# Kernel tuning notes

Hardware: AMD Instinct MI355X
Metric: run time of the kernel (lower is better)

Reference implementation:

```python
import jax, jax.numpy as jnp
import numpy as np

B = 4096
N_FEAT = 4
VOCAB = 100000
EMB = 64
N_NEG = 3
TEMP = 1.0
EPS = 1e-8  # torch.cosine_similarity eps


def setup_inputs() -> dict:
    key = jax.random.key(0)
    ks = jax.random.split(key, 12)
    inp = {}
    inp['user_ids'] = jax.random.randint(ks[0], (B, N_FEAT), 0, VOCAB)
    inp['item_ids'] = jax.random.randint(ks[1], (B, N_FEAT), 0, VOCAB)
    inp['sw_ids'] = jax.random.randint(ks[2], (B,), 0, VOCAB)
    inp['user_tables'] = jax.random.normal(ks[3], (N_FEAT, VOCAB, EMB), jnp.float32) * 0.05
    inp['item_tables'] = jax.random.normal(ks[4], (N_FEAT, VOCAB, EMB), jnp.float32) * 0.05
    # sample weights must be positive (log is taken)
    inp['sw_table'] = jax.random.uniform(ks[5], (VOCAB,), jnp.float32) * 0.99 + 0.01
    inp['uW1'] = jax.random.normal(ks[6], (256, 256), jnp.float32) * 0.05
    inp['ub1'] = jnp.zeros((256,), jnp.float32)
    inp['uW2'] = jax.random.normal(ks[7], (256, 128), jnp.float32) * 0.05
    inp['ub2'] = jnp.zeros((128,), jnp.float32)
    inp['iW1'] = jax.random.normal(ks[8], (256, 256), jnp.float32) * 0.05
    inp['ib1'] = jnp.zeros((256,), jnp.float32)
    inp['iW2'] = jax.random.normal(ks[9], (256, 128), jnp.float32) * 0.05
    inp['ib2'] = jnp.zeros((128,), jnp.float32)
    return inp


def _embed(tables, ids):
    # tables: [F, V, E], ids: [B, F] -> [B, F*E]
    e = jax.vmap(lambda tbl, idx: tbl[idx], in_axes=(0, 1))(tables, ids)  # [F, B, E]
    return jnp.transpose(e, (1, 0, 2)).reshape(ids.shape[0], -1)


def _mlp(x, W1, b1, W2, b2):
    # torch-rechub MLP with output_layer=False: activation after every layer
    h = jax.nn.relu(x @ W1 + b1)
    return jax.nn.relu(h @ W2 + b2)


def reference(user_ids, item_ids, sw_ids, user_tables, item_tables, sw_table,
              uW1, ub1, uW2, ub2, iW1, ib1, iW2, ib2):
    u = _mlp(_embed(user_tables, user_ids), uW1, ub1, uW2, ub2)   # [B, 128]
    v = _mlp(_embed(item_tables, item_ids), iW1, ib1, iW2, ib2)   # [B, 128]
    un = u / jnp.maximum(jnp.linalg.norm(u, axis=-1, keepdims=True), EPS)
    vn = v / jnp.maximum(jnp.linalg.norm(v, axis=-1, keepdims=True), EPS)
    pred = un @ vn.T                                              # [B, B] cosine sim
    sw = sw_table[sw_ids]                                         # [B]
    scores = pred - jnp.log(sw)[None, :]                          # debias per item column
    # in-batch negative sampling: row i pairs with cols (i..i+n_neg) mod B
    rows = jnp.repeat(jnp.arange(B), N_NEG + 1)
    cols = ((jnp.arange(B)[:, None] + jnp.arange(N_NEG + 1)[None, :]) % B).reshape(-1)
    out = scores[rows, cols] / TEMP
    return out.reshape(B, N_NEG + 1)
```

## Files before the change

kernel.cpp:

```cpp
#include <hip/hip_runtime.h>
#include <math.h>

#define BATCH 4096
#define NFEAT 4
#define VOCAB 100000
#define EMB 64
#define D_IN 256
#define D_H 256
#define D_O 128

__global__ __launch_bounds__(256) void gather_kernel(
    const int* __restrict__ user_ids, const int* __restrict__ item_ids,
    const float* __restrict__ user_tables, const float* __restrict__ item_tables,
    float* __restrict__ Xu, float* __restrict__ Xi) {
  int tid = blockIdx.x * blockDim.x + threadIdx.x;
  int which = tid / (BATCH * 64);
  int r = tid % (BATCH * 64);
  int b = r >> 6;
  int c4 = r & 63;
  int f = c4 >> 4;
  int e4 = c4 & 15;
  const int* ids = which ? item_ids : user_ids;
  const float* tbl = which ? item_tables : user_tables;
  float* X = which ? Xi : Xu;
  int id = ids[b * NFEAT + f];
  const float4* src = (const float4*)(tbl + ((size_t)f * VOCAB + (size_t)id) * EMB);
  ((float4*)(X + (size_t)b * D_IN))[c4] = src[e4];
}

__global__ __launch_bounds__(256) void gemm_bias_relu(
    const float* __restrict__ Au, const float* __restrict__ Ai,
    const float* __restrict__ Wu, const float* __restrict__ Wi,
    const float* __restrict__ bu, const float* __restrict__ bi,
    float* __restrict__ Cu, float* __restrict__ Ci, int K, int N) {
  const float* A; const float* W; const float* bias; float* C;
  if (blockIdx.z == 0) { A = Au; W = Wu; bias = bu; C = Cu; }
  else                 { A = Ai; W = Wi; bias = bi; C = Ci; }

  __shared__ float As[16][68];
  __shared__ float Bs[16][68];

  const int m0 = blockIdx.x * 64;
  const int n0 = blockIdx.y * 64;
  const int tid = threadIdx.x;
  const int tx = tid & 15;
  const int ty = tid >> 4;

  float acc[4][4] = {};

  for (int k0 = 0; k0 < K; k0 += 16) {
    {
      int row = tid >> 2, kq = tid & 3;
      float4 a = *(const float4*)(A + (size_t)(m0 + row) * K + k0 + kq * 4);
      As[kq * 4 + 0][row] = a.x;
      As[kq * 4 + 1][row] = a.y;
      As[kq * 4 + 2][row] = a.z;
      As[kq * 4 + 3][row] = a.w;
    }
    {
      int kc = tid >> 4, nq = tid & 15;
      float4 b = *(const float4*)(W + (size_t)(k0 + kc) * N + n0 + nq * 4);
      *(float4*)(&Bs[kc][nq * 4]) = b;
    }
    __syncthreads();
#pragma unroll
    for (int kc = 0; kc < 16; kc++) {
      float4 a = *(const float4*)(&As[kc][ty * 4]);
      float4 b = *(const float4*)(&Bs[kc][tx * 4]);
      float av[4] = {a.x, a.y, a.z, a.w};
      float bv[4] = {b.x, b.y, b.z, b.w};
#pragma unroll
      for (int i = 0; i < 4; i++)
#pragma unroll
        for (int j = 0; j < 4; j++) acc[i][j] += av[i] * bv[j];
    }
    __syncthreads();
  }

#pragma unroll
  for (int i = 0; i < 4; i++) {
    int m = m0 + ty * 4 + i;
#pragma unroll
    for (int j = 0; j < 4; j++) {
      int n = n0 + tx * 4 + j;
      float v = acc[i][j] + bias[n];
      C[(size_t)m * N + n] = v > 0.f ? v : 0.f;
    }
  }
}

__global__ __launch_bounds__(256) void score_kernel(
    const float* __restrict__ U, const float* __restrict__ V,
    const int* __restrict__ sw_ids, const float* __restrict__ sw_table,
    float* __restrict__ out) {
  int wave = threadIdx.x >> 6;
  int lane = threadIdx.x & 63;
  int i = blockIdx.x * 4 + wave;

  float u0 = U[(size_t)i * 128 + lane];
  float u1 = U[(size_t)i * 128 + 64 + lane];
  float nu = u0 * u0 + u1 * u1;
#pragma unroll
  for (int off = 32; off; off >>= 1) nu += __shfl_xor(nu, off);
  nu = fmaxf(sqrtf(nu), 1e-8f);

#pragma unroll
  for (int j = 0; j < 4; j++) {
    int c = (i + j) & (BATCH - 1);
    float v0 = V[(size_t)c * 128 + lane];
    float v1 = V[(size_t)c * 128 + 64 + lane];
    float d = u0 * v0 + u1 * v1;
    float nv = v0 * v0 + v1 * v1;
#pragma unroll
    for (int off = 32; off; off >>= 1) {
      d += __shfl_xor(d, off);
      nv += __shfl_xor(nv, off);
    }
    nv = fmaxf(sqrtf(nv), 1e-8f);
    if (lane == 0) {
      float sw = sw_table[sw_ids[c]];
      out[(size_t)i * 4 + j] = d / (nu * nv) - logf(sw);
    }
  }
}

extern "C" void kernel_launch(void* const* d_in, const int* in_sizes, int n_in,
                              void* d_out, int out_size, void* d_ws, size_t ws_size,
                              hipStream_t stream) {
  (void)in_sizes; (void)n_in; (void)out_size; (void)ws_size;
  const int*   user_ids    = (const int*)d_in[0];
  const int*   item_ids    = (const int*)d_in[1];
  const int*   sw_ids      = (const int*)d_in[2];
  const float* user_tables = (const float*)d_in[3];
  const float* item_tables = (const float*)d_in[4];
  const float* sw_table    = (const float*)d_in[5];
  const float* uW1 = (const float*)d_in[6];
  const float* ub1 = (const float*)d_in[7];
  const float* uW2 = (const float*)d_in[8];
  const float* ub2 = (const float*)d_in[9];
  const float* iW1 = (const float*)d_in[10];
  const float* ib1 = (const float*)d_in[11];
  const float* iW2 = (const float*)d_in[12];
  const float* ib2 = (const float*)d_in[13];
  float* out = (float*)d_out;

  float* Xu = (float*)d_ws;
  float* Xi = Xu + (size_t)BATCH * D_IN;
  float* Hu = Xi + (size_t)BATCH * D_IN;
  float* Hi = Hu + (size_t)BATCH * D_H;
  float* U  = Hi + (size_t)BATCH * D_H;
  float* V  = U  + (size_t)BATCH * D_O;

  gather_kernel<<<(2 * BATCH * 64) / 256, 256, 0, stream>>>(
      user_ids, item_ids, user_tables, item_tables, Xu, Xi);

  gemm_bias_relu<<<dim3(BATCH / 64, D_H / 64, 2), 256, 0, stream>>>(
      Xu, Xi, uW1, iW1, ub1, ib1, Hu, Hi, D_IN, D_H);

  gemm_bias_relu<<<dim3(BATCH / 64, D_O / 64, 2), 256, 0, stream>>>(
      Hu, Hi, uW2, iW2, ub2, ib2, U, V, D_H, D_O);

  score_kernel<<<BATCH / 4, 256, 0, stream>>>(U, V, sw_ids, sw_table, out);
}
```

Measured before the change: 244.5 us.

## Fuse embedding gather and both MLP layers into one per-tower kernel

Replaces the separate gather kernel and two tiled GEMM kernels with a single tower kernel. Each block gathers 32 rows of embeddings into shared memory, runs layer 1 into a shared hidden buffer, then runs layer 2 and writes L2-normalized outputs. The score kernel drops its norm computations because U and V arrive normalized. This removes the global round trips for X and H and two launches. In exchange, each block rereads W1 and W2 from global or L2 memory, and only 256 blocks are launched.

New measurement: 272.7 us. 11.6% more time.

```diff
diff --git a/kernel.cpp b/kernel.cpp
--- a/kernel.cpp
+++ b/kernel.cpp
@@ -8,83 +8,120 @@
 #define D_IN 256
 #define D_H 256
 #define D_O 128
+#define ROWS 32
 
-__global__ __launch_bounds__(256) void gather_kernel(
+__global__ __launch_bounds__(256) void tower_kernel(
     const int* __restrict__ user_ids, const int* __restrict__ item_ids,
     const float* __restrict__ user_tables, const float* __restrict__ item_tables,
-    float* __restrict__ Xu, float* __restrict__ Xi) {
-  int tid = blockIdx.x * blockDim.x + threadIdx.x;
-  int which = tid / (BATCH * 64);
-  int r = tid % (BATCH * 64);
-  int b = r >> 6;
-  int c4 = r & 63;
-  int f = c4 >> 4;
-  int e4 = c4 & 15;
-  const int* ids = which ? item_ids : user_ids;
-  const float* tbl = which ? item_tables : user_tables;
-  float* X = which ? Xi : Xu;
-  int id = ids[b * NFEAT + f];
-  const float4* src = (const float4*)(tbl + ((size_t)f * VOCAB + (size_t)id) * EMB);
-  ((float4*)(X + (size_t)b * D_IN))[c4] = src[e4];
-}
+    const float* __restrict__ uW1, const float* __restrict__ ub1,
+    const float* __restrict__ uW2, const float* __restrict__ ub2,
+    const float* __restrict__ iW1, const float* __restrict__ ib1,
+    const float* __restrict__ iW2, const float* __restrict__ ib2,
+    float* __restrict__ U, float* __restrict__ V) {
+  const int tower = blockIdx.y;
+  const int* ids = tower ? item_ids : user_ids;
+  const float* tab = tower ? item_tables : user_tables;
+  const float* W1 = tower ? iW1 : uW1;
+  const float* b1 = tower ? ib1 : ub1;
+  const float* W2 = tower ? iW2 : uW2;
+  const float* b2 = tower ? ib2 : ub2;
+  float* O = tower ? V : U;
 
-__global__ __launch_bounds__(256) void gemm_bias_relu(
-    const float* __restrict__ Au, const float* __restrict__ Ai,
-    const float* __restrict__ Wu, const float* __restrict__ Wi,
-    const float* __restrict__ bu, const float* __restrict__ bi,
-    float* __restrict__ Cu, float* __restrict__ Ci, int K, int N) {
-  const float* A; const float* W; const float* bias; float* C;
-  if (blockIdx.z == 0) { A = Au; W = Wu; bias = bu; C = Cu; }
-  else                 { A = Ai; W = Wi; bias = bi; C = Ci; }
+  const int r0 = blockIdx.x * ROWS;
+  const int tid = threadIdx.x;
 
-  __shared__ float As[16][68];
-  __shared__ float Bs[16][68];
-
-  const int m0 = blockIdx.x * 64;
-  const int n0 = blockIdx.y * 64;
-  const int tid = threadIdx.x;
-  const int tx = tid & 15;
-  const int ty = tid >> 4;
-
-  float acc[4][4] = {};
-
-  for (int k0 = 0; k0 < K; k0 += 16) {
-    {
-      int row = tid >> 2, kq = tid & 3;
-      float4 a = *(const float4*)(A + (size_t)(m0 + row) * K + k0 + kq * 4);
-      As[kq * 4 + 0][row] = a.x;
-      As[kq * 4 + 1][row] = a.y;
-      As[kq * 4 + 2][row] = a.z;
-      As[kq * 4 + 3][row] = a.w;
-    }
-    {
-      int kc = tid >> 4, nq = tid & 15;
-      float4 b = *(const float4*)(W + (size_t)(k0 + kc) * N + n0 + nq * 4);
-      *(float4*)(&Bs[kc][nq * 4]) = b;
-    }
-    __syncthreads();
-#pragma unroll
-    for (int kc = 0; kc < 16; kc++) {
-      float4 a = *(const float4*)(&As[kc][ty * 4]);
-      float4 b = *(const float4*)(&Bs[kc][tx * 4]);
-      float av[4] = {a.x, a.y, a.z, a.w};
-      float bv[4] = {b.x, b.y, b.z, b.w};
-#pragma unroll
-      for (int i = 0; i < 4; i++)
-#pragma unroll
-        for (int j = 0; j < 4; j++) acc[i][j] += av[i] * bv[j];
-    }
-    __syncthreads();
-  }
+  __shared__ float Xs[ROWS][D_IN];
+  __shared__ float Hs[ROWS][D_H];
 
 #pragma unroll
-  for (int i = 0; i < 4; i++) {
-    int m = m0 + ty * 4 + i;
+  for (int i = 0; i < 8; i++) {
+    int slot = i * 256 + tid;
+    int row = slot >> 6;
+    int c4 = slot & 63;
+    int f = c4 >> 4;
+    int id = ids[(size_t)(r0 + row) * NFEAT + f];
+    const float4* src = (const float4*)(tab + ((size_t)f * VOCAB + (size_t)id) * EMB);
+    *(float4*)&Xs[row][c4 * 4] = src[c4 & 15];
+  }
+  __syncthreads();
+
+  const int tx = tid & 63;
+  const int w = tid >> 6;
+
+  {
+    const int c0 = tx * 4;
+    float acc[8][4];
+    float4 bb = *(const float4*)(b1 + c0);
 #pragma unroll
-    for (int j = 0; j < 4; j++) {
-      int n = n0 + tx * 4 + j;
-      float v = acc[i][j] + bias[n];
-      C[(size_t)m * N + n] = v > 0.f ? v : 0.f;
+    for (int r = 0; r < 8; r++) {
+      acc[r][0] = bb.x; acc[r][1] = bb.y; acc[r][2] = bb.z; acc[r][3] = bb.w;
+    }
+    for (int k = 0; k < D_IN; k += 4) {
+      float4 wv[4];
+#pragma unroll
+      for (int kk = 0; kk < 4; kk++)
+        wv[kk] = *(const float4*)(W1 + (size_t)(k + kk) * D_H + c0);
+      float4 xv[8];
+#pragma unroll
+      for (int r = 0; r < 8; r++)
+        xv[r] = *(const float4*)&Xs[w * 8 + r][k];
+#pragma unroll
+      for (int r = 0; r < 8; r++) {
+        const float* xp = (const float*)&xv[r];
+#pragma unroll
+        for (int kk = 0; kk < 4; kk++) {
+          const float* wp = (const float*)&wv[kk];
+          float a = xp[kk];
+#pragma unroll
+          for (int j = 0; j < 4; j++) acc[r][j] += a * wp[j];
+        }
+      }
+    }
+#pragma unroll
+    for (int r = 0; r < 8; r++) {
+      float4 o;
+      o.x = fmaxf(acc[r][0], 0.f); o.y = fmaxf(acc[r][1], 0.f);
+      o.z = fmaxf(acc[r][2], 0.f); o.w = fmaxf(acc[r][3], 0.f);
+      *(float4*)&Hs[w * 8 + r][c0] = o;
+    }
+  }
+  __syncthreads();
+
+  {
+    const int c0 = tx * 2;
+    float acc[8][2];
+    float2 bb = *(const float2*)(b2 + c0);
+#pragma unroll
+    for (int r = 0; r < 8; r++) { acc[r][0] = bb.x; acc[r][1] = bb.y; }
+    for (int k = 0; k < D_H; k += 4) {
+      float2 wv[4];
+#pragma unroll
+      for (int kk = 0; kk < 4; kk++)
+        wv[kk] = *(const float2*)(W2 + (size_t)(k + kk) * D_O + c0);
+      float4 xv[8];
+#pragma unroll
+      for (int r = 0; r < 8; r++)
+        xv[r] = *(const float4*)&Hs[w * 8 + r][k];
+#pragma unroll
+      for (int r = 0; r < 8; r++) {
+        const float* xp = (const float*)&xv[r];
+#pragma unroll
+        for (int kk = 0; kk < 4; kk++) {
+          acc[r][0] += xp[kk] * wv[kk].x;
+          acc[r][1] += xp[kk] * wv[kk].y;
+        }
+      }
+    }
+#pragma unroll
+    for (int r = 0; r < 8; r++) {
+      float y0 = fmaxf(acc[r][0], 0.f);
+      float y1 = fmaxf(acc[r][1], 0.f);
+      float s = y0 * y0 + y1 * y1;
+#pragma unroll
+      for (int off = 32; off; off >>= 1) s += __shfl_xor(s, off);
+      float inv = 1.f / fmaxf(sqrtf(s), 1e-8f);
+      float2 o; o.x = y0 * inv; o.y = y1 * inv;
+      *(float2*)(O + (size_t)(r0 + w * 8 + r) * D_O + c0) = o;
     }
   }
 }
@@ -97,29 +134,19 @@
   int lane = threadIdx.x & 63;
   int i = blockIdx.x * 4 + wave;
 
-  float u0 = U[(size_t)i * 128 + lane];
-  float u1 = U[(size_t)i * 128 + 64 + lane];
-  float nu = u0 * u0 + u1 * u1;
-#pragma unroll
-  for (int off = 32; off; off >>= 1) nu += __shfl_xor(nu, off);
-  nu = fmaxf(sqrtf(nu), 1e-8f);
+  float u0 = U[(size_t)i * D_O + lane];
+  float u1 = U[(size_t)i * D_O + 64 + lane];
 
 #pragma unroll
   for (int j = 0; j < 4; j++) {
     int c = (i + j) & (BATCH - 1);
-    float v0 = V[(size_t)c * 128 + lane];
-    float v1 = V[(size_t)c * 128 + 64 + lane];
+    float v0 = V[(size_t)c * D_O + lane];
+    float v1 = V[(size_t)c * D_O + 64 + lane];
     float d = u0 * v0 + u1 * v1;
-    float nv = v0 * v0 + v1 * v1;
 #pragma unroll
-    for (int off = 32; off; off >>= 1) {
-      d += __shfl_xor(d, off);
-      nv += __shfl_xor(nv, off);
-    }
-    nv = fmaxf(sqrtf(nv), 1e-8f);
+    for (int off = 32; off; off >>= 1) d += __shfl_xor(d, off);
     if (lane == 0) {
-      float sw = sw_table[sw_ids[c]];
-      out[(size_t)i * 4 + j] = d / (nu * nv) - logf(sw);
+      out[(size_t)i * 4 + j] = d - logf(sw_table[sw_ids[c]]);
     }
   }
 }
@@ -144,21 +171,12 @@
   const float* ib2 = (const float*)d_in[13];
   float* out = (float*)d_out;
 
-  float* Xu = (float*)d_ws;
-  float* Xi = Xu + (size_t)BATCH * D_IN;
-  float* Hu = Xi + (size_t)BATCH * D_IN;
-  float* Hi = Hu + (size_t)BATCH * D_H;
-  float* U  = Hi + (size_t)BATCH * D_H;
-  float* V  = U  + (size_t)BATCH * D_O;
+  float* U = (float*)d_ws;
+  float* V = U + (size_t)BATCH * D_O;
 
-  gather_kernel<<<(2 * BATCH * 64) / 256, 256, 0, stream>>>(
-      user_ids, item_ids, user_tables, item_tables, Xu, Xi);
-
-  gemm_bias_relu<<<dim3(BATCH / 64, D_H / 64, 2), 256, 0, stream>>>(
-      Xu, Xi, uW1, iW1, ub1, ib1, Hu, Hi, D_IN, D_H);
-
-  gemm_bias_relu<<<dim3(BATCH / 64, D_O / 64, 2), 256, 0, stream>>>(
-      Hu, Hi, uW2, iW2, ub2, ib2, U, V, D_H, D_O);
+  tower_kernel<<<dim3(BATCH / ROWS, 2), 256, 0, stream>>>(
+      user_ids, item_ids, user_tables, item_tables,
+      uW1, ub1, uW2, ub2, iW1, ib1, iW2, ib2, U, V);
 
   score_kernel<<<BATCH / 4, 256, 0, stream>>>(U, V, sw_ids, sw_table, out);
 }
```
